# Kernel tuning notes

Hardware: AMD Instinct MI355X
Metric: run time of the kernel (lower is better)

The kernel has to match this reference:

```python
import jax, jax.numpy as jnp
import numpy as np

TOP_K = 2


def setup_inputs() -> dict:
    key = jax.random.key(0)
    k1, k2 = jax.random.split(key)
    x = jax.random.normal(k1, (4, 4096, 2048), dtype=jnp.float32)
    W = jax.random.normal(k2, (64, 2048), dtype=jnp.float32) * (1.0 / np.sqrt(2048))
    return {"x": x, "W": W}


def reference(x, W):
    B, S, D = x.shape
    E = W.shape[0]
    # logits: [B*S, E] via linear router (no bias)
    flat = x.reshape(-1, D)
    logits = jnp.einsum('td,ed->te', flat, W)
    probs = jax.nn.softmax(logits, axis=-1)
    # eval path: top-k indices
    _, top_k_indices = jax.lax.top_k(probs, TOP_K)          # [T, K]
    # scatter 1s -> mask; scatter gathered probs -> router_probs (== probs*mask)
    router_mask = jax.nn.one_hot(top_k_indices, E, dtype=probs.dtype).sum(axis=-2)  # [T, E]
    router_probs = probs * router_mask
    # normalize (top_k > 1: gradient flows through the sum)
    router_probs = router_probs / router_probs.sum(axis=-1, keepdims=True)
    return (router_mask.reshape(B, S, E),
            top_k_indices.reshape(B, S, TOP_K),
            router_probs.reshape(B, S, E),
            probs.reshape(B, S, E))
```

## Files before the change

kernel.cpp:

```cpp
#include <hip/hip_runtime.h>
#include <math.h>


#define D_DIM 2048
#define E_DIM 64

typedef __bf16 bf16x8 __attribute__((ext_vector_type(8)));
typedef unsigned short us8 __attribute__((ext_vector_type(8)));
typedef float f32x4 __attribute__((ext_vector_type(4)));

static __device__ __forceinline__ unsigned short f2bf(float f) {
    unsigned int u = __float_as_uint(f);
    u += 0x7fffu + ((u >> 16) & 1u);
    return (unsigned short)(u >> 16);
}
static __device__ __forceinline__ float bf2f(unsigned short h) {
    return __uint_as_float(((unsigned int)h) << 16);
}
static __device__ __forceinline__ void split4(const float4 v, ushort4* h, ushort4* l) {
    h->x = f2bf(v.x); l->x = f2bf(v.x - bf2f(h->x));
    h->y = f2bf(v.y); l->y = f2bf(v.y - bf2f(h->y));
    h->z = f2bf(v.z); l->z = f2bf(v.z - bf2f(h->z));
    h->w = f2bf(v.w); l->w = f2bf(v.w - bf2f(h->w));
}

static __device__ __forceinline__ void gld_lds16(const void* g, void* l) {
    __builtin_amdgcn_global_load_lds(
        (const __attribute__((address_space(1))) unsigned int*)g,
        (__attribute__((address_space(3))) unsigned int*)l,
        16, 0, 0);
}

__global__ __launch_bounds__(256, 1) void convert_w(
    const float4* __restrict__ W4, unsigned short* __restrict__ WH,
    unsigned short* __restrict__ WL)
{
    int i = blockIdx.x * 256 + threadIdx.x;
    float4 v = W4[i];
    ushort4 h, l;
    split4(v, &h, &l);
    *(ushort4*)&WH[i * 4] = h;
    *(ushort4*)&WL[i * 4] = l;
}

template<int KS>
__global__ __launch_bounds__(256, 4) void gemm_part(
    const float* __restrict__ x,
    const unsigned short* __restrict__ WHg, const unsigned short* __restrict__ WLg,
    float* __restrict__ P, int T)
{
    __shared__ __align__(16) float          XF [64 * 64];
    __shared__ __align__(16) unsigned short WHs[64 * 64];
    __shared__ __align__(16) unsigned short WLs[64 * 64];

    const int tid  = threadIdx.x;
    const int lane = tid & 63;
    const int wv   = tid >> 6;
    const int quad = lane >> 4;
    const int l16  = lane & 15;

    const int ntb = T >> 6;
    const int tb  = blockIdx.x % ntb;
    const int ksl = blockIdx.x / ntb;
    const int t0  = tb << 6;
    const int NCH = (D_DIM / KS) >> 6;
    const int k0  = ksl * (D_DIM / KS);

    f32x4 acc[4];
    #pragma unroll
    for (int n = 0; n < 4; ++n) { f32x4 z = {0.f, 0.f, 0.f, 0.f}; acc[n] = z; }

    const int srow = wv * 4 + (lane >> 4);
    const int scg  = lane & 15;
    const int we   = wv * 8 + (lane >> 3);
    const int wo   = lane & 7;

    for (int ch = 0; ch < NCH; ++ch) {
        const int kc = k0 + (ch << 6);

        #pragma unroll
        for (int i = 0; i < 4; ++i) {
            int row = i * 16 + srow;
            int cg  = scg ^ (row & 15);
            gld_lds16(x + (size_t)(t0 + row) * D_DIM + kc + cg * 4,
                      &XF[(i * 256 + wv * 64) * 4]);
        }
        #pragma unroll
        for (int i2 = 0; i2 < 2; ++i2) {
            int e  = i2 * 32 + we;
            int og = wo ^ (e & 7);
            gld_lds16(WHg + (size_t)e * D_DIM + kc + og * 8,
                      &WHs[(i2 * 256 + wv * 64) * 8]);
            gld_lds16(WLg + (size_t)e * D_DIM + kc + og * 8,
                      &WLs[(i2 * 256 + wv * 64) * 8]);
        }
        __syncthreads();

        #pragma unroll
        for (int ks = 0; ks < 2; ++ks) {
            const int tr = wv * 16 + l16;
            const int c0 = ks * 8 + quad * 2;
            float4 xa = *(const float4*)&XF[(tr * 16 + ( c0      ^ (tr & 15))) * 4];
            float4 xb = *(const float4*)&XF[(tr * 16 + ((c0 + 1) ^ (tr & 15))) * 4];
            ushort4 h0, l0, h1, l1;
            split4(xa, &h0, &l0);
            split4(xb, &h1, &l1);
            union { us8 u; bf16x8 b; } ua, ul;
            ua.u = (us8){h0.x, h0.y, h0.z, h0.w, h1.x, h1.y, h1.z, h1.w};
            ul.u = (us8){l0.x, l0.y, l0.z, l0.w, l1.x, l1.y, l1.z, l1.w};

            #pragma unroll
            for (int n = 0; n < 4; ++n) {
                int e = n * 16 + l16;
                int o = ks * 4 + quad;
                int s = e * 8 + (o ^ (e & 7));
                bf16x8 bh = *(const bf16x8*)&WHs[s * 8];
                bf16x8 bl = *(const bf16x8*)&WLs[s * 8];
                acc[n] = __builtin_amdgcn_mfma_f32_16x16x32_bf16(ua.b, bh, acc[n], 0, 0, 0);
                acc[n] = __builtin_amdgcn_mfma_f32_16x16x32_bf16(ul.b, bh, acc[n], 0, 0, 0);
                acc[n] = __builtin_amdgcn_mfma_f32_16x16x32_bf16(ua.b, bl, acc[n], 0, 0, 0);
            }
        }
        __syncthreads();
    }

    float* Pb = P + ((size_t)ksl * T + t0) * 64;
    #pragma unroll
    for (int n = 0; n < 4; ++n)
        #pragma unroll
        for (int r = 0; r < 4; ++r)
            Pb[(wv * 16 + quad * 4 + r) * 64 + n * 16 + l16] = acc[n][r];
}

template<int KS>
__global__ __launch_bounds__(256, 4) void reduce_router(
    const float* __restrict__ P, int T,
    float* __restrict__ mask_out, float* __restrict__ idx_out,
    float* __restrict__ rp_out, float* __restrict__ probs_out)
{
    const int tid  = threadIdx.x;
    const int lane = tid & 63;
    const int wv   = tid >> 6;

    for (int i = 0; i < 4; ++i) {
        int t = blockIdx.x * 16 + wv * 4 + i;
        float v = 0.f;
        #pragma unroll
        for (int s = 0; s < KS; ++s)
            v += P[((size_t)s * T + t) * 64 + lane];

        float bv = v; int bi = lane;
        #pragma unroll
        for (int off = 1; off < 64; off <<= 1) {
            float ov = __shfl_xor(bv, off, 64);
            int   oi = __shfl_xor(bi, off, 64);
            bool take = (ov > bv) || (ov == bv && oi < bi);
            bv = take ? ov : bv;
            bi = take ? oi : bi;
        }
        float m = bv; int i1 = bi;

        float p = __expf(v - m);
        float s = p;
        #pragma unroll
        for (int off = 1; off < 64; off <<= 1) s += __shfl_xor(s, off, 64);
        float prob = p / s;

        float v2 = (lane == i1) ? -INFINITY : v;
        float bv2 = v2; int bi2 = lane;
        #pragma unroll
        for (int off = 1; off < 64; off <<= 1) {
            float ov = __shfl_xor(bv2, off, 64);
            int   oi = __shfl_xor(bi2, off, 64);
            bool take = (ov > bv2) || (ov == bv2 && oi < bi2);
            bv2 = take ? ov : bv2;
            bi2 = take ? oi : bi2;
        }
        int i2 = bi2;

        float pd = __shfl(prob, i1, 64) + __shfl(prob, i2, 64);
        bool top = (lane == i1) || (lane == i2);

        mask_out[(size_t)t * 64 + lane]  = top ? 1.f : 0.f;
        rp_out[(size_t)t * 64 + lane]    = top ? prob / pd : 0.f;
        probs_out[(size_t)t * 64 + lane] = prob;
        if (lane == 0) {
            idx_out[(size_t)t * 2]     = (float)i1;
            idx_out[(size_t)t * 2 + 1] = (float)i2;
        }
    }
}

extern "C" void kernel_launch(void* const* d_in, const int* in_sizes, int n_in,
                              void* d_out, int out_size, void* d_ws, size_t ws_size,
                              hipStream_t stream) {
    const float* x = (const float*)d_in[0];
    const float* W = (const float*)d_in[1];
    float* out = (float*)d_out;

    const int T  = in_sizes[0] / D_DIM;
    const int WN = in_sizes[1];

    unsigned short* WH = (unsigned short*)d_ws;
    unsigned short* WL = WH + WN;
    float* P = (float*)(WL + WN);

    float* mask_out  = out;
    float* idx_out   = out + (size_t)T * E_DIM;
    float* rp_out    = idx_out + (size_t)T * 2;
    float* probs_out = rp_out + (size_t)T * E_DIM;

    const size_t avail = ws_size - (size_t)WN * 4;
    const size_t slice_bytes = (size_t)T * 64 * 4;

    convert_w<<<dim3(WN / 1024), dim3(256), 0, stream>>>((const float4*)W, WH, WL);

    if (avail >= 4 * slice_bytes) {
        gemm_part<4><<<dim3((T / 64) * 4), dim3(256), 0, stream>>>(x, WH, WL, P, T);
        reduce_router<4><<<dim3(T / 16), dim3(256), 0, stream>>>(
            P, T, mask_out, idx_out, rp_out, probs_out);
    } else if (avail >= 2 * slice_bytes) {
        gemm_part<2><<<dim3((T / 64) * 2), dim3(256), 0, stream>>>(x, WH, WL, P, T);
        reduce_router<2><<<dim3(T / 16), dim3(256), 0, stream>>>(
            P, T, mask_out, idx_out, rp_out, probs_out);
    } else {
        gemm_part<1><<<dim3(T / 64), dim3(256), 0, stream>>>(x, WH, WL, P, T);
        reduce_router<1><<<dim3(T / 16), dim3(256), 0, stream>>>(
            P, T, mask_out, idx_out, rp_out, probs_out);
    }
}
```

Measured before the change: 208.3 us.

## Double-buffer x tiles in LDS and load W fragments directly into registers

The x tile is now double-buffered in LDS, so the load for the next chunk is issued before computing the current one, with a partial vmcnt wait and raw barriers replacing __syncthreads. The W hi/lo bf16 fragments are no longer staged through LDS; each lane loads its 16-byte fragments straight from global memory (L2-resident) into registers. The goal is to overlap global latency with MFMA work and cut LDS traffic. The costs are more registers (launch bounds lowered to 3 waves), a hand-tuned vmcnt count that must match the number of outstanding loads, and a wrapped prefetch on the last chunk that loads data it never uses.

```diff
diff --git a/kernel.cpp b/kernel.cpp
--- a/kernel.cpp
+++ b/kernel.cpp
@@ -44,14 +44,12 @@
 }
 
 template<int KS>
-__global__ __launch_bounds__(256, 4) void gemm_part(
+__global__ __launch_bounds__(256, 3) void gemm_part(
     const float* __restrict__ x,
     const unsigned short* __restrict__ WHg, const unsigned short* __restrict__ WLg,
     float* __restrict__ P, int T)
 {
-    __shared__ __align__(16) float          XF [64 * 64];
-    __shared__ __align__(16) unsigned short WHs[64 * 64];
-    __shared__ __align__(16) unsigned short WLs[64 * 64];
+    __shared__ __align__(16) float XF[2][64 * 64];
 
     const int tid  = threadIdx.x;
     const int lane = tid & 63;
@@ -72,36 +70,50 @@
 
     const int srow = wv * 4 + (lane >> 4);
     const int scg  = lane & 15;
-    const int we   = wv * 8 + (lane >> 3);
-    const int wo   = lane & 7;
+
+    #pragma unroll
+    for (int i = 0; i < 4; ++i) {
+        int row = i * 16 + srow;
+        int cg  = scg ^ (row & 15);
+        gld_lds16(x + (size_t)(t0 + row) * D_DIM + k0 + cg * 4,
+                  &XF[0][(i * 256 + wv * 64) * 4]);
+    }
 
     for (int ch = 0; ch < NCH; ++ch) {
-        const int kc = k0 + (ch << 6);
-
-        #pragma unroll
-        for (int i = 0; i < 4; ++i) {
-            int row = i * 16 + srow;
-            int cg  = scg ^ (row & 15);
-            gld_lds16(x + (size_t)(t0 + row) * D_DIM + kc + cg * 4,
-                      &XF[(i * 256 + wv * 64) * 4]);
-        }
-        #pragma unroll
-        for (int i2 = 0; i2 < 2; ++i2) {
-            int e  = i2 * 32 + we;
-            int og = wo ^ (e & 7);
-            gld_lds16(WHg + (size_t)e * D_DIM + kc + og * 8,
-                      &WHs[(i2 * 256 + wv * 64) * 8]);
-            gld_lds16(WLg + (size_t)e * D_DIM + kc + og * 8,
-                      &WLs[(i2 * 256 + wv * 64) * 8]);
-        }
-        __syncthreads();
-
-        #pragma unroll
-        for (int ks = 0; ks < 2; ++ks) {
+        const int buf = ch & 1;
+        const int kc  = k0 + (ch << 6);
+
+        bf16x8 bh[2][4], bl[2][4];
+        #pragma unroll
+        for (int ks2 = 0; ks2 < 2; ++ks2)
+            #pragma unroll
+            for (int n = 0; n < 4; ++n) {
+                const size_t wo = (size_t)(n * 16 + l16) * D_DIM + kc + ks2 * 32 + quad * 8;
+                bh[ks2][n] = *(const bf16x8*)(WHg + wo);
+                bl[ks2][n] = *(const bf16x8*)(WLg + wo);
+            }
+
+        {
+            const int chn = (ch + 1) & (NCH - 1);
+            const int kcn = k0 + (chn << 6);
+            #pragma unroll
+            for (int i = 0; i < 4; ++i) {
+                int row = i * 16 + srow;
+                int cg  = scg ^ (row & 15);
+                gld_lds16(x + (size_t)(t0 + row) * D_DIM + kcn + cg * 4,
+                          &XF[buf ^ 1][(i * 256 + wv * 64) * 4]);
+            }
+        }
+
+        asm volatile("s_waitcnt vmcnt(20)" ::: "memory");
+        __builtin_amdgcn_s_barrier();
+
+        #pragma unroll
+        for (int ks2 = 0; ks2 < 2; ++ks2) {
             const int tr = wv * 16 + l16;
-            const int c0 = ks * 8 + quad * 2;
-            float4 xa = *(const float4*)&XF[(tr * 16 + ( c0      ^ (tr & 15))) * 4];
-            float4 xb = *(const float4*)&XF[(tr * 16 + ((c0 + 1) ^ (tr & 15))) * 4];
+            const int c0 = ks2 * 8 + quad * 2;
+            float4 xa = *(const float4*)&XF[buf][(tr * 16 + ( c0      ^ (tr & 15))) * 4];
+            float4 xb = *(const float4*)&XF[buf][(tr * 16 + ((c0 + 1) ^ (tr & 15))) * 4];
             ushort4 h0, l0, h1, l1;
             split4(xa, &h0, &l0);
             split4(xb, &h1, &l1);
@@ -111,17 +123,13 @@
 
             #pragma unroll
             for (int n = 0; n < 4; ++n) {
-                int e = n * 16 + l16;
-                int o = ks * 4 + quad;
-                int s = e * 8 + (o ^ (e & 7));
-                bf16x8 bh = *(const bf16x8*)&WHs[s * 8];
-                bf16x8 bl = *(const bf16x8*)&WLs[s * 8];
-                acc[n] = __builtin_amdgcn_mfma_f32_16x16x32_bf16(ua.b, bh, acc[n], 0, 0, 0);
-                acc[n] = __builtin_amdgcn_mfma_f32_16x16x32_bf16(ul.b, bh, acc[n], 0, 0, 0);
-                acc[n] = __builtin_amdgcn_mfma_f32_16x16x32_bf16(ua.b, bl, acc[n], 0, 0, 0);
+                acc[n] = __builtin_amdgcn_mfma_f32_16x16x32_bf16(ua.b, bh[ks2][n], acc[n], 0, 0, 0);
+                acc[n] = __builtin_amdgcn_mfma_f32_16x16x32_bf16(ul.b, bh[ks2][n], acc[n], 0, 0, 0);
+                acc[n] = __builtin_amdgcn_mfma_f32_16x16x32_bf16(ua.b, bl[ks2][n], acc[n], 0, 0, 0);
             }
         }
-        __syncthreads();
+
+        __builtin_amdgcn_s_barrier();
     }
 
     float* Pb = P + ((size_t)ksl * T + t0) * 64;
```

Result: slower. 229.0 us (+10.0%).
